# Kernel optimization log

Hardware: AMD Instinct MI355X
Metric: run time of the kernel (lower is better)

The kernel has to match this reference:

```python
import jax, jax.numpy as jnp
import numpy as np

TOPK = 2048


def setup_inputs() -> dict:
    key = jax.random.key(0)
    ks = jax.random.split(key, 16)
    M = 20000
    boxes = jax.random.uniform(ks[0], (M, 4), dtype=jnp.float32)
    scores = jax.random.uniform(ks[1], (M,), dtype=jnp.float32)
    classes = jax.random.randint(ks[2], (M,), 0, 80, dtype=jnp.int64)
    def lin(k, fan_in, fan_out):
        b = 1.0 / np.sqrt(fan_in)
        kw, kb = jax.random.split(k)
        w = jax.random.uniform(kw, (fan_in, fan_out), jnp.float32, -b, b)
        bias = jax.random.uniform(kb, (fan_out,), jnp.float32, -b, b)
        return w, bias
    sup_w1, sup_b1 = lin(ks[3], 7, 32)
    sup_w2, sup_b2 = lin(ks[4], 32, 16)
    sup_w3, sup_b3 = lin(ks[5], 16, 1)
    lam_w1, lam_b1 = lin(ks[6], 5, 16)
    lam_w2, lam_b2 = lin(ks[7], 16, 1)
    return {
        'boxes': boxes, 'scores': scores, 'classes': classes,
        'sup_w1': sup_w1, 'sup_b1': sup_b1, 'sup_w2': sup_w2, 'sup_b2': sup_b2,
        'sup_w3': sup_w3, 'sup_b3': sup_b3,
        'lam_w1': lam_w1, 'lam_b1': lam_b1, 'lam_w2': lam_w2, 'lam_b2': lam_b2,
    }


def _box_iou(b):
    # b: [N,4] in (x, y, w, h)
    x, y, w, h = b[:, 0], b[:, 1], b[:, 2], b[:, 3]
    area = w * h
    ix1 = jnp.maximum(x[:, None], x[None, :])
    iy1 = jnp.maximum(y[:, None], y[None, :])
    ix2 = jnp.minimum((x + w)[:, None], (x + w)[None, :])
    iy2 = jnp.minimum((y + h)[:, None], (y + h)[None, :])
    inter = jnp.clip(ix2 - ix1, 0) * jnp.clip(iy2 - iy1, 0)
    union = area[:, None] + area[None, :] - inter
    return inter / (union + 1e-06)


def _dacs(boxes, scores, classes,
          sup_w1, sup_b1, sup_w2, sup_b2, sup_w3, sup_b3,
          lam_w1, lam_b1, lam_w2, lam_b2):
    k = min(TOPK, scores.shape[0])
    top_scores, idx = jax.lax.top_k(scores, k)
    b = boxes[idx]            # [N,4]
    cls = classes[idx]        # [N]
    N = k
    iou = _box_iou(b)         # [N,N]
    D = iou.mean(axis=1)      # [N]
    x, y, w, h = b[:, 0], b[:, 1], b[:, 2], b[:, 3]
    feats = jnp.stack([
        iou,
        jnp.abs(x[:, None] - x[None, :]),
        jnp.abs(y[:, None] - y[None, :]),
        jnp.abs(w[:, None] - w[None, :]),
        jnp.abs(h[:, None] - h[None, :]),
        jnp.broadcast_to(top_scores[:, None], (N, N)),
        jnp.broadcast_to(top_scores[None, :], (N, N)),
    ], axis=-1)               # [N,N,7]
    hdn = jax.nn.relu(feats @ sup_w1 + sup_b1)       # [N,N,32]
    hdn = jax.nn.relu(hdn @ sup_w2 + sup_b2)         # [N,N,16]
    s_ij = jax.nn.sigmoid((hdn @ sup_w3 + sup_b3)[..., 0])  # [N,N]
    class_mask = (cls[:, None] == cls[None, :]).astype(s_ij.dtype)
    s_ij = s_ij * class_mask
    lam_in = jnp.concatenate([b, top_scores[:, None]], axis=1)  # [N,5]
    lam_h = jax.nn.relu(lam_in @ lam_w1 + lam_b1)
    lam = jax.nn.sigmoid((lam_h @ lam_w2 + lam_b2)[:, 0])       # [N]
    S = jnp.sum(s_ij * iou, axis=1)
    E = lam * S * D
    new_scores = top_scores * jnp.exp(-E)
    return b, new_scores, cls


def reference(boxes, scores, classes,
              sup_w1, sup_b1, sup_w2, sup_b2, sup_w3, sup_b3,
              lam_w1, lam_b1, lam_w2, lam_b2):
    return _dacs(boxes, scores, classes,
                 sup_w1, sup_b1, sup_w2, sup_b2, sup_w3, sup_b3,
                 lam_w1, lam_b1, lam_w2, lam_b2)
```

## Files before the change

### kernel.cpp

```cpp
#include <hip/hip_runtime.h>
#include <math.h>

#define TOPK 2048
#define NCLS 80
#define NBIN 4096
#define CMAX 2560
#define K1B  32
#define STN  1024
#define CTN  256
#define CROWS 2

struct SelP {
    const float* scores; const float* boxes; const int* classes;
    int M; int K;
    float4* sel_box; float* sel_score; int* sel_cls;
    int* cstart;
    short* clist;
};

struct CmpP {
    const float4* sel_box; const float* sel_score; const int* sel_cls;
    const int* cstart; const short* clist;
    const float* sw1; const float* sb1; const float* sw2; const float* sb2;
    const float* sw3; const float* sb3;
    const float* lw1; const float* lb1; const float* lw2; const float* lb2;
    int K;
    float* out_boxes; float* out_scores; float* out_cls;
};

__device__ __forceinline__ float iou_of(float xi, float yi, float ai,
                                        float x2i, float y2i, float4 bj) {
    float ix1 = fmaxf(xi, bj.x), iy1 = fmaxf(yi, bj.y);
    float ix2 = fminf(x2i, bj.x + bj.z), iy2 = fminf(y2i, bj.y + bj.w);
    float iw = fmaxf(ix2 - ix1, 0.0f), ih = fmaxf(iy2 - iy1, 0.0f);
    float inter = iw * ih;
    float uni = ai + bj.z * bj.w - inter;
    return inter / (uni + 1e-6f);
}

__device__ __forceinline__ int digest12(float s) {
    int v = (int)(s * 4096.0f);
    return v < 0 ? 0 : (v > NBIN - 1 ? NBIN - 1 : v);
}

__device__ __forceinline__ float key_score(unsigned long long kk) {
    unsigned mono = (unsigned)(kk >> 32);
    unsigned ob = (mono & 0x80000000u) ? (mono & 0x7FFFFFFFu) : ~mono;
    return __uint_as_float(ob);
}

__global__ __launch_bounds__(STN, 1) void k_sel(SelP p) {
    __shared__ int   bincur[NBIN];
    __shared__ int   binbase[NBIN];
    __shared__ unsigned long long skeys[CMAX];
    __shared__ int   sfx[STN];
    __shared__ int   wsum[STN / 64];
    __shared__ int   sh_cT;
    __shared__ int   cls_of[CMAX];
    __shared__ int   rk_of[CMAX];
    __shared__ int   ccnt[NCLS], ccur[NCLS];
    __shared__ int   wtot;

    int tid = threadIdx.x, bid = blockIdx.x;
    int M = p.M, K = p.K, M4 = M >> 2;
    bool prep = (bid == 0);

    for (int b = tid; b < NBIN; b += STN) bincur[b] = 0;
    if (tid < NCLS) ccnt[tid] = 0;
    __syncthreads();

    const float4* s4p = (const float4*)p.scores;
    for (int i4 = tid; i4 < M4; i4 += STN) {
        float4 v = s4p[i4];
        atomicAdd(&bincur[digest12(v.x)], 1);
        atomicAdd(&bincur[digest12(v.y)], 1);
        atomicAdd(&bincur[digest12(v.z)], 1);
        atomicAdd(&bincur[digest12(v.w)], 1);
    }
    for (int i = M4 * 4 + tid; i < M; i += STN)
        atomicAdd(&bincur[digest12(p.scores[i])], 1);
    __syncthreads();

    {
        const int BPT = NBIN / STN;
        int c0 = tid * BPT, sum = 0;
        #pragma unroll
        for (int u = 0; u < BPT; u++) sum += bincur[c0 + u];
        int lane = tid & 63;
        int x = sum;
        #pragma unroll
        for (int off = 1; off < 64; off <<= 1) {
            int v = __shfl_down(x, off, 64);
            if (lane + off < 64) x += v;
        }
        if (lane == 0) wsum[tid >> 6] = x;
        __syncthreads();
        if (tid < STN / 64) {
            int t = wsum[tid];
            #pragma unroll
            for (int off = 1; off < STN / 64; off <<= 1) {
                int v = __shfl_down(t, off, 64);
                if (tid + off < STN / 64) t += v;
            }
            wsum[tid] = t;
        }
        __syncthreads();
        int wid = tid >> 6;
        int higher = (wid < STN / 64 - 1) ? wsum[wid + 1] : 0;
        sfx[tid] = x + higher;
    }
    __syncthreads();

    {
        const int BPT = NBIN / STN;
        int running = (tid < STN - 1) ? sfx[tid + 1] : 0;
        int c0 = tid * BPT;
        for (int u = BPT - 1; u >= 0; u--) {
            int b = c0 + u, cnt = bincur[b];
            binbase[b] = running;
            if (running < K && running + cnt >= K) sh_cT = b;
            running += cnt;
        }
    }
    __syncthreads();
    int cT = sh_cT;
    for (int b = tid; b < NBIN; b += STN) bincur[b] = binbase[b];
    __syncthreads();

    for (int i4 = tid; i4 < M4; i4 += STN) {
        float4 v = s4p[i4];
        #pragma unroll
        for (int u = 0; u < 4; u++) {
            float s = (u == 0) ? v.x : (u == 1) ? v.y : (u == 2) ? v.z : v.w;
            int d = digest12(s);
            if (d >= cT) {
                int i = i4 * 4 + u;
                int slot = atomicAdd(&bincur[d], 1);
                if (slot < CMAX) {
                    unsigned b = __float_as_uint(s);
                    b = (b & 0x80000000u) ? ~b : (b | 0x80000000u);
                    skeys[slot] = ((unsigned long long)b << 32) |
                                  (unsigned long long)(0xFFFFFFFFu - (unsigned)i);
                }
            }
        }
    }
    for (int i = M4 * 4 + tid; i < M; i += STN) {
        float s = p.scores[i];
        int d = digest12(s);
        if (d >= cT) {
            int slot = atomicAdd(&bincur[d], 1);
            if (slot < CMAX) {
                unsigned b = __float_as_uint(s);
                b = (b & 0x80000000u) ? ~b : (b | 0x80000000u);
                skeys[slot] = ((unsigned long long)b << 32) |
                              (unsigned long long)(0xFFFFFFFFu - (unsigned)i);
            }
        }
    }
    __syncthreads();

    int C = bincur[cT]; if (C > CMAX) C = CMAX;
    {
        const float4* boxes4 = (const float4*)p.boxes;
        for (int s = tid; s < C; s += STN) {
            unsigned long long ks = skeys[s];
            unsigned idx = 0xFFFFFFFFu - (unsigned)(ks & 0xFFFFFFFFull);
            bool mine = ((int)(idx & (K1B - 1)) == bid);
            if (!prep && !mine) continue;
            float sc = key_score(ks);
            int d = digest12(sc);
            int st = binbase[d], en = bincur[d]; if (en > CMAX) en = CMAX;
            int r = binbase[d];
            for (int t = st; t < en; t++) r += (skeys[t] > ks) ? 1 : 0;
            bool ok = (r < K);
            int c = -1;
            if (ok) c = p.classes[idx];
            if (prep) {
                cls_of[s] = ok ? c : -1;
                rk_of[s] = r;
                if (ok) atomicAdd(&ccnt[c], 1);
            }
            if (mine && ok) {
                p.sel_box[r] = boxes4[idx];
                p.sel_score[r] = sc;
                p.sel_cls[r] = c;
            }
        }
    }
    __syncthreads();

    if (prep) {
        int x = 0, v = 0;
        if (tid < 128) {
            v = (tid < NCLS) ? ccnt[tid] : 0;
            x = v;
            #pragma unroll
            for (int off = 1; off < 64; off <<= 1) {
                int t = __shfl_up(x, off, 64);
                if ((tid & 63) >= off) x += t;
            }
            if (tid == 63) wtot = x;
        }
        __syncthreads();
        if (tid < NCLS) {
            int excl = x - v + ((tid >= 64) ? wtot : 0);
            ccur[tid] = excl;
            p.cstart[tid] = excl;
        }
        if (tid == 0) p.cstart[NCLS] = K;
        __syncthreads();
        for (int s = tid; s < C; s += STN) {
            int c = cls_of[s];
            if (c >= 0) {
                int pos = atomicAdd(&ccur[c], 1);
                p.clist[pos] = (short)rk_of[s];
            }
        }
    }
}

__global__ __launch_bounds__(CTN, 2) void k_cmp(CmpP p) {
    __shared__ float swt[914];
    __shared__ float wpart[8];
    __shared__ int   rowc[CROWS];
    __shared__ int   prefix[CROWS + 1];
    __shared__ float Ssum[CROWS], Drow[CROWS];

    int tid = threadIdx.x, bid = blockIdx.x;
    int K = p.K;
    int r0 = bid * CROWS;
    int nrows = K - r0; if (nrows > CROWS) nrows = CROWS;
    if (nrows <= 0) return;

    for (int t = tid; t < 224; t += CTN) swt[t] = p.sw1[t];
    if (tid < 32) swt[224 + tid] = p.sb1[tid];
    for (int t = tid; t < 512; t += CTN) swt[256 + t] = p.sw2[t];
    if (tid < 16) swt[768 + tid] = p.sb2[tid];
    if (tid < 16) swt[784 + tid] = p.sw3[tid];
    if (tid == 0) swt[800] = p.sb3[0];
    if (tid < 80) swt[801 + tid] = p.lw1[tid];
    if (tid < 16) swt[881 + tid] = p.lb1[tid];
    if (tid < 16) swt[897 + tid] = p.lw2[tid];
    if (tid == 0) swt[913] = p.lb2[0];

    if (tid < CROWS) {
        Ssum[tid] = 0.0f;
        int st = 0, cnt = 0;
        if (tid < nrows) {
            int c = p.sel_cls[r0 + tid];
            st = p.cstart[c];
            cnt = p.cstart[c + 1] - st;
        }
        rowc[tid] = st;
        prefix[tid] = cnt;
    }
    __syncthreads();
    if (tid == 0) {
        int a0 = prefix[0], a1 = prefix[1];
        prefix[0] = 0; prefix[1] = a0; prefix[2] = a0 + a1;
    }

    {
        float4 bi0 = p.sel_box[r0];
        float4 bi1 = (nrows > 1) ? p.sel_box[r0 + 1] : bi0;
        float a0 = bi0.z * bi0.w, x20 = bi0.x + bi0.z, y20 = bi0.y + bi0.w;
        float a1 = bi1.z * bi1.w, x21 = bi1.x + bi1.z, y21 = bi1.y + bi1.w;
        float d0 = 0.0f, d1 = 0.0f;
        for (int j = tid; j < K; j += CTN) {
            float4 bj = p.sel_box[j];
            d0 += iou_of(bi0.x, bi0.y, a0, x20, y20, bj);
            d1 += iou_of(bi1.x, bi1.y, a1, x21, y21, bj);
        }
        #pragma unroll
        for (int off = 32; off >= 1; off >>= 1) {
            d0 += __shfl_xor(d0, off, 64);
            d1 += __shfl_xor(d1, off, 64);
        }
        int lane = tid & 63, wv = tid >> 6;
        if (lane == 0) { wpart[wv * 2] = d0; wpart[wv * 2 + 1] = d1; }
    }
    __syncthreads();
    if (tid < nrows)
        Drow[tid] = (wpart[tid] + wpart[2 + tid] + wpart[4 + tid] + wpart[6 + tid])
                    / (float)K;

    int Pb = prefix[CROWS];
    const float* W1 = swt;       const float* B1 = swt + 224;
    const float* W2 = swt + 256; const float* B2 = swt + 768;
    const float* W3 = swt + 784; float B3 = swt[800];

    for (int pp = tid; pp < Pb; pp += CTN) {
        int row = (pp >= prefix[1]) ? 1 : 0;
        int j = (int)p.clist[rowc[row] + (pp - prefix[row])];
        float4 bi = p.sel_box[r0 + row];
        float4 bj = p.sel_box[j];
        float ai = bi.z * bi.w, x2i = bi.x + bi.z, y2i = bi.y + bi.w;
        float iou = iou_of(bi.x, bi.y, ai, x2i, y2i, bj);
        float f1 = fabsf(bi.x - bj.x), f2 = fabsf(bi.y - bj.y);
        float f3 = fabsf(bi.z - bj.z), f4 = fabsf(bi.w - bj.w);
        float f5 = p.sel_score[r0 + row], f6 = p.sel_score[j];
        float acc2[16];
        #pragma unroll
        for (int q = 0; q < 16; q++) acc2[q] = B2[q];
        #pragma unroll 2
        for (int o = 0; o < 32; o++) {
            float a = B1[o];
            a += iou * W1[0 * 32 + o];
            a += f1 * W1[1 * 32 + o];
            a += f2 * W1[2 * 32 + o];
            a += f3 * W1[3 * 32 + o];
            a += f4 * W1[4 * 32 + o];
            a += f5 * W1[5 * 32 + o];
            a += f6 * W1[6 * 32 + o];
            float h = fmaxf(a, 0.0f);
            #pragma unroll
            for (int q = 0; q < 16; q++) acc2[q] += h * W2[o * 16 + q];
        }
        float acc3 = B3;
        #pragma unroll
        for (int q = 0; q < 16; q++) acc3 += fmaxf(acc2[q], 0.0f) * W3[q];
        atomicAdd(&Ssum[row], iou / (1.0f + expf(-acc3)));
    }
    __syncthreads();

    if (tid < nrows) {
        int r = r0 + tid;
        float4 bi = p.sel_box[r];
        float si = p.sel_score[r];
        const float* LW1 = swt + 801; const float* LB1 = swt + 881;
        const float* LW2 = swt + 897; float LB2 = swt[913];
        float in5[5] = { bi.x, bi.y, bi.z, bi.w, si };
        float acc = LB2;
        #pragma unroll
        for (int o = 0; o < 16; o++) {
            float a2 = LB1[o];
            #pragma unroll
            for (int f = 0; f < 5; f++) a2 += in5[f] * LW1[f * 16 + o];
            acc += fmaxf(a2, 0.0f) * LW2[o];
        }
        float lam = 1.0f / (1.0f + expf(-acc));
        ((float4*)p.out_boxes)[r] = bi;
        p.out_cls[r] = (float)p.sel_cls[r];
        p.out_scores[r] = si * expf(-lam * Ssum[tid] * Drow[tid]);
    }
}

extern "C" void kernel_launch(void* const* d_in, const int* in_sizes, int n_in,
                              void* d_out, int out_size, void* d_ws, size_t ws_size,
                              hipStream_t stream) {
    int M = in_sizes[1];
    int K = (M < TOPK) ? M : TOPK;

    char* ws = (char*)d_ws;
    float4* sel_box   = (float4*)ws;           ws += (size_t)TOPK * 16;
    float*  sel_score = (float*)ws;            ws += (size_t)TOPK * 4;
    int*    sel_cls   = (int*)ws;              ws += (size_t)TOPK * 4;
    int*    cstart    = (int*)ws;              ws += (size_t)(NCLS + 2) * 4;
    short*  clist     = (short*)ws;            ws += (size_t)TOPK * 2;

    SelP sp;
    sp.scores  = (const float*)d_in[1];
    sp.boxes   = (const float*)d_in[0];
    sp.classes = (const int*)d_in[2];
    sp.M = M; sp.K = K;
    sp.sel_box = sel_box; sp.sel_score = sel_score; sp.sel_cls = sel_cls;
    sp.cstart = cstart; sp.clist = clist;

    CmpP cp;
    cp.sel_box = sel_box; cp.sel_score = sel_score; cp.sel_cls = sel_cls;
    cp.cstart = cstart; cp.clist = clist;
    cp.sw1 = (const float*)d_in[3];  cp.sb1 = (const float*)d_in[4];
    cp.sw2 = (const float*)d_in[5];  cp.sb2 = (const float*)d_in[6];
    cp.sw3 = (const float*)d_in[7];  cp.sb3 = (const float*)d_in[8];
    cp.lw1 = (const float*)d_in[9];  cp.lb1 = (const float*)d_in[10];
    cp.lw2 = (const float*)d_in[11]; cp.lb2 = (const float*)d_in[12];
    cp.K = K;
    cp.out_boxes  = (float*)d_out;
    cp.out_scores = (float*)d_out + (size_t)K * 4;
    cp.out_cls    = (float*)d_out + (size_t)K * 5;

    k_sel<<<K1B, STN, 0, stream>>>(sp);
    k_cmp<<<(K + CROWS - 1) / CROWS, CTN, 0, stream>>>(cp);
}
```

Measured before the change: 106.8 us.

## Collapse top-k selection to one block and process four rows per compute block

```diff
diff --git a/kernel.cpp b/kernel.cpp
--- a/kernel.cpp
+++ b/kernel.cpp
@@ -5,21 +5,20 @@
 #define NCLS 80
 #define NBIN 4096
 #define CMAX 2560
-#define K1B  32
-#define STN  1024
-#define CTN  256
-#define CROWS 2
+#define TNS  1024
+#define TND  512
+#define CROWS 4
 
 struct SelP {
     const float* scores; const float* boxes; const int* classes;
     int M; int K;
-    float4* sel_box; float* sel_score; int* sel_cls;
+    float4* selB; float* selS; int* selC;
     int* cstart;
     short* clist;
 };
 
 struct CmpP {
-    const float4* sel_box; const float* sel_score; const int* sel_cls;
+    const float4* selB; const float* selS; const int* selC;
     const int* cstart; const short* clist;
     const float* sw1; const float* sb1; const float* sw2; const float* sb2;
     const float* sw3; const float* sb3;
@@ -43,46 +42,50 @@
     return v < 0 ? 0 : (v > NBIN - 1 ? NBIN - 1 : v);
 }
 
+__device__ __forceinline__ unsigned long long make_key(float s, unsigned i) {
+    unsigned b = __float_as_uint(s);
+    b = (b & 0x80000000u) ? ~b : (b | 0x80000000u);
+    return ((unsigned long long)b << 32) |
+           (unsigned long long)(0xFFFFFFFFu - i);
+}
+
 __device__ __forceinline__ float key_score(unsigned long long kk) {
     unsigned mono = (unsigned)(kk >> 32);
     unsigned ob = (mono & 0x80000000u) ? (mono & 0x7FFFFFFFu) : ~mono;
     return __uint_as_float(ob);
 }
 
-__global__ __launch_bounds__(STN, 1) void k_sel(SelP p) {
+__global__ __launch_bounds__(TNS, 1) void k_sel(SelP p) {
     __shared__ int   bincur[NBIN];
-    __shared__ int   binbase[NBIN];
     __shared__ unsigned long long skeys[CMAX];
-    __shared__ int   sfx[STN];
-    __shared__ int   wsum[STN / 64];
+    __shared__ int   sfx[TNS];
+    __shared__ int   wsum[TNS / 64];
     __shared__ int   sh_cT;
-    __shared__ int   cls_of[CMAX];
-    __shared__ int   rk_of[CMAX];
+    __shared__ short scls[TOPK];
     __shared__ int   ccnt[NCLS], ccur[NCLS];
     __shared__ int   wtot;
 
-    int tid = threadIdx.x, bid = blockIdx.x;
+    int tid = threadIdx.x;
     int M = p.M, K = p.K, M4 = M >> 2;
-    bool prep = (bid == 0);
-
-    for (int b = tid; b < NBIN; b += STN) bincur[b] = 0;
+
+    for (int b = tid; b < NBIN; b += TNS) bincur[b] = 0;
     if (tid < NCLS) ccnt[tid] = 0;
     __syncthreads();
 
     const float4* s4p = (const float4*)p.scores;
-    for (int i4 = tid; i4 < M4; i4 += STN) {
+    for (int i4 = tid; i4 < M4; i4 += TNS) {
         float4 v = s4p[i4];
         atomicAdd(&bincur[digest12(v.x)], 1);
         atomicAdd(&bincur[digest12(v.y)], 1);
         atomicAdd(&bincur[digest12(v.z)], 1);
         atomicAdd(&bincur[digest12(v.w)], 1);
     }
-    for (int i = M4 * 4 + tid; i < M; i += STN)
+    for (int i = M4 * 4 + tid; i < M; i += TNS)
         atomicAdd(&bincur[digest12(p.scores[i])], 1);
     __syncthreads();
 
     {
-        const int BPT = NBIN / STN;
+        const int BPT = NBIN / TNS;
         int c0 = tid * BPT, sum = 0;
         #pragma unroll
         for (int u = 0; u < BPT; u++) sum += bincur[c0 + u];
@@ -95,102 +98,89 @@
         }
         if (lane == 0) wsum[tid >> 6] = x;
         __syncthreads();
-        if (tid < STN / 64) {
+        if (tid < TNS / 64) {
             int t = wsum[tid];
             #pragma unroll
-            for (int off = 1; off < STN / 64; off <<= 1) {
+            for (int off = 1; off < TNS / 64; off <<= 1) {
                 int v = __shfl_down(t, off, 64);
-                if (tid + off < STN / 64) t += v;
+                if (tid + off < TNS / 64) t += v;
             }
             wsum[tid] = t;
         }
         __syncthreads();
         int wid = tid >> 6;
-        int higher = (wid < STN / 64 - 1) ? wsum[wid + 1] : 0;
+        int higher = (wid < TNS / 64 - 1) ? wsum[wid + 1] : 0;
         sfx[tid] = x + higher;
     }
     __syncthreads();
 
     {
-        const int BPT = NBIN / STN;
-        int running = (tid < STN - 1) ? sfx[tid + 1] : 0;
+        const int BPT = NBIN / TNS;
+        int running = (tid < TNS - 1) ? sfx[tid + 1] : 0;
         int c0 = tid * BPT;
         for (int u = BPT - 1; u >= 0; u--) {
             int b = c0 + u, cnt = bincur[b];
-            binbase[b] = running;
             if (running < K && running + cnt >= K) sh_cT = b;
+            bincur[b] = (running << 16);
             running += cnt;
         }
     }
     __syncthreads();
     int cT = sh_cT;
-    for (int b = tid; b < NBIN; b += STN) bincur[b] = binbase[b];
-    __syncthreads();
-
-    for (int i4 = tid; i4 < M4; i4 += STN) {
+
+    for (int i4 = tid; i4 < M4; i4 += TNS) {
         float4 v = s4p[i4];
         #pragma unroll
         for (int u = 0; u < 4; u++) {
             float s = (u == 0) ? v.x : (u == 1) ? v.y : (u == 2) ? v.z : v.w;
             int d = digest12(s);
             if (d >= cT) {
-                int i = i4 * 4 + u;
-                int slot = atomicAdd(&bincur[d], 1);
-                if (slot < CMAX) {
-                    unsigned b = __float_as_uint(s);
-                    b = (b & 0x80000000u) ? ~b : (b | 0x80000000u);
-                    skeys[slot] = ((unsigned long long)b << 32) |
-                                  (unsigned long long)(0xFFFFFFFFu - (unsigned)i);
-                }
+                int old = atomicAdd(&bincur[d], 1);
+                int slot = (old >> 16) + (old & 0xFFFF);
+                if (slot < CMAX)
+                    skeys[slot] = make_key(s, (unsigned)(i4 * 4 + u));
             }
         }
     }
-    for (int i = M4 * 4 + tid; i < M; i += STN) {
+    for (int i = M4 * 4 + tid; i < M; i += TNS) {
         float s = p.scores[i];
         int d = digest12(s);
         if (d >= cT) {
-            int slot = atomicAdd(&bincur[d], 1);
-            if (slot < CMAX) {
-                unsigned b = __float_as_uint(s);
-                b = (b & 0x80000000u) ? ~b : (b | 0x80000000u);
-                skeys[slot] = ((unsigned long long)b << 32) |
-                              (unsigned long long)(0xFFFFFFFFu - (unsigned)i);
-            }
-        }
-    }
-    __syncthreads();
-
-    int C = bincur[cT]; if (C > CMAX) C = CMAX;
+            int old = atomicAdd(&bincur[d], 1);
+            int slot = (old >> 16) + (old & 0xFFFF);
+            if (slot < CMAX) skeys[slot] = make_key(s, (unsigned)i);
+        }
+    }
+    __syncthreads();
+
+    int pkT = bincur[cT];
+    int C = (pkT >> 16) + (pkT & 0xFFFF); if (C > CMAX) C = CMAX;
     {
         const float4* boxes4 = (const float4*)p.boxes;
-        for (int s = tid; s < C; s += STN) {
+        for (int s = tid; s < C; s += TNS) {
             unsigned long long ks = skeys[s];
             unsigned idx = 0xFFFFFFFFu - (unsigned)(ks & 0xFFFFFFFFull);
-            bool mine = ((int)(idx & (K1B - 1)) == bid);
-            if (!prep && !mine) continue;
             float sc = key_score(ks);
             int d = digest12(sc);
-            int st = binbase[d], en = bincur[d]; if (en > CMAX) en = CMAX;
-            int r = binbase[d];
+            int pk = bincur[d];
+            int st = pk >> 16;
+            int en = st + (pk & 0xFFFF); if (en > CMAX) en = CMAX;
+            int r = st;
             for (int t = st; t < en; t++) r += (skeys[t] > ks) ? 1 : 0;
-            bool ok = (r < K);
-            int c = -1;
-            if (ok) c = p.classes[idx];
-            if (prep) {
-                cls_of[s] = ok ? c : -1;
-                rk_of[s] = r;
-                if (ok) atomicAdd(&ccnt[c], 1);
+            if (r < K) {
+                int c = p.classes[idx];
+                p.selB[r] = boxes4[idx];
+                p.selS[r] = sc;
+                p.selC[r] = c;
+                scls[r] = (short)c;
             }
-            if (mine && ok) {
-                p.sel_box[r] = boxes4[idx];
-                p.sel_score[r] = sc;
-                p.sel_cls[r] = c;
-            }
-        }
-    }
-    __syncthreads();
-
-    if (prep) {
+        }
+    }
+    __syncthreads();
+
+    for (int r = tid; r < K; r += TNS) atomicAdd(&ccnt[scls[r]], 1);
+    __syncthreads();
+    {
         int x = 0, v = 0;
         if (tid < 128) {
             v = (tid < NCLS) ? ccnt[tid] : 0;
@@ -210,19 +200,16 @@
         }
         if (tid == 0) p.cstart[NCLS] = K;
         __syncthreads();
-        for (int s = tid; s < C; s += STN) {
-            int c = cls_of[s];
-            if (c >= 0) {
-                int pos = atomicAdd(&ccur[c], 1);
-                p.clist[pos] = (short)rk_of[s];
-            }
-        }
-    }
-}
-
-__global__ __launch_bounds__(CTN, 2) void k_cmp(CmpP p) {
+        for (int r = tid; r < K; r += TNS) {
+            int pos = atomicAdd(&ccur[scls[r]], 1);
+            p.clist[pos] = (short)r;
+        }
+    }
+}
+
+__global__ __launch_bounds__(TND, 4) void k_cmp(CmpP p) {
     __shared__ float swt[914];
-    __shared__ float wpart[8];
+    __shared__ float wpart[(TND / 64) * CROWS];
     __shared__ int   rowc[CROWS];
     __shared__ int   prefix[CROWS + 1];
     __shared__ float Ssum[CROWS], Drow[CROWS];
@@ -233,9 +220,9 @@
     int nrows = K - r0; if (nrows > CROWS) nrows = CROWS;
     if (nrows <= 0) return;
 
-    for (int t = tid; t < 224; t += CTN) swt[t] = p.sw1[t];
+    for (int t = tid; t < 224; t += TND) swt[t] = p.sw1[t];
     if (tid < 32) swt[224 + tid] = p.sb1[tid];
-    for (int t = tid; t < 512; t += CTN) swt[256 + t] = p.sw2[t];
+    for (int t = tid; t < 512; t += TND) swt[256 + t] = p.sw2[t];
     if (tid < 16) swt[768 + tid] = p.sb2[tid];
     if (tid < 16) swt[784 + tid] = p.sw3[tid];
     if (tid == 0) swt[800] = p.sb3[0];
@@ -248,7 +235,7 @@
         Ssum[tid] = 0.0f;
         int st = 0, cnt = 0;
         if (tid < nrows) {
-            int c = p.sel_cls[r0 + tid];
+            int c = p.selC[r0 + tid];
             st = p.cstart[c];
             cnt = p.cstart[c + 1] - st;
         }
@@ -257,49 +244,67 @@
     }
     __syncthreads();
     if (tid == 0) {
-        int a0 = prefix[0], a1 = prefix[1];
-        prefix[0] = 0; prefix[1] = a0; prefix[2] = a0 + a1;
-    }
-
-    {
-        float4 bi0 = p.sel_box[r0];
-        float4 bi1 = (nrows > 1) ? p.sel_box[r0 + 1] : bi0;
-        float a0 = bi0.z * bi0.w, x20 = bi0.x + bi0.z, y20 = bi0.y + bi0.w;
-        float a1 = bi1.z * bi1.w, x21 = bi1.x + bi1.z, y21 = bi1.y + bi1.w;
-        float d0 = 0.0f, d1 = 0.0f;
-        for (int j = tid; j < K; j += CTN) {
-            float4 bj = p.sel_box[j];
-            d0 += iou_of(bi0.x, bi0.y, a0, x20, y20, bj);
-            d1 += iou_of(bi1.x, bi1.y, a1, x21, y21, bj);
+        int acc = 0;
+        #pragma unroll
+        for (int rr = 0; rr < CROWS; rr++) { int t = prefix[rr]; prefix[rr] = acc; acc += t; }
+        prefix[CROWS] = acc;
+    }
+
+    {
+        float4 b0 = p.selB[r0];
+        float4 b1 = (nrows > 1) ? p.selB[r0 + 1] : b0;
+        float4 b2 = (nrows > 2) ? p.selB[r0 + 2] : b0;
+        float4 b3 = (nrows > 3) ? p.selB[r0 + 3] : b0;
+        float a0 = b0.z * b0.w, x20 = b0.x + b0.z, y20 = b0.y + b0.w;
+        float a1 = b1.z * b1.w, x21 = b1.x + b1.z, y21 = b1.y + b1.w;
+        float a2 = b2.z * b2.w, x22 = b2.x + b2.z, y22 = b2.y + b2.w;
+        float a3 = b3.z * b3.w, x23 = b3.x + b3.z, y23 = b3.y + b3.w;
+        float d0 = 0.0f, d1 = 0.0f, d2 = 0.0f, d3 = 0.0f;
+        for (int j = tid; j < K; j += TND) {
+            float4 bj = p.selB[j];
+            d0 += iou_of(b0.x, b0.y, a0, x20, y20, bj);
+            d1 += iou_of(b1.x, b1.y, a1, x21, y21, bj);
+            d2 += iou_of(b2.x, b2.y, a2, x22, y22, bj);
+            d3 += iou_of(b3.x, b3.y, a3, x23, y23, bj);
         }
         #pragma unroll
         for (int off = 32; off >= 1; off >>= 1) {
             d0 += __shfl_xor(d0, off, 64);
             d1 += __shfl_xor(d1, off, 64);
+            d2 += __shfl_xor(d2, off, 64);
+            d3 += __shfl_xor(d3, off, 64);
         }
         int lane = tid & 63, wv = tid >> 6;
-        if (lane == 0) { wpart[wv * 2] = d0; wpart[wv * 2 + 1] = d1; }
-    }
-    __syncthreads();
-    if (tid < nrows)
-        Drow[tid] = (wpart[tid] + wpart[2 + tid] + wpart[4 + tid] + wpart[6 + tid])
-                    / (float)K;
+        if (lane == 0) {
+            wpart[wv * CROWS + 0] = d0;
+            wpart[wv * CROWS + 1] = d1;
+            wpart[wv * CROWS + 2] = d2;
+            wpart[wv * CROWS + 3] = d3;
+        }
+    }
+    __syncthreads();
+    if (tid < nrows) {
+        float s = 0.0f;
+        #pragma unroll
+        for (int wv = 0; wv < TND / 64; wv++) s += wpart[wv * CROWS + tid];
+        Drow[tid] = s / (float)K;
+    }
 
     int Pb = prefix[CROWS];
     const float* W1 = swt;       const float* B1 = swt + 224;
     const float* W2 = swt + 256; const float* B2 = swt + 768;
     const float* W3 = swt + 784; float B3 = swt[800];
 
-    for (int pp = tid; pp < Pb; pp += CTN) {
-        int row = (pp >= prefix[1]) ? 1 : 0;
+    for (int pp = tid; pp < Pb; pp += TND) {
+        int row = (pp >= prefix[1]) + (pp >= prefix[2]) + (pp >= prefix[3]);
         int j = (int)p.clist[rowc[row] + (pp - prefix[row])];
-        float4 bi = p.sel_box[r0 + row];
-        float4 bj = p.sel_box[j];
+        float4 bi = p.selB[r0 + row];
+        float4 bj = p.selB[j];
         float ai = bi.z * bi.w, x2i = bi.x + bi.z, y2i = bi.y + bi.w;
         float iou = iou_of(bi.x, bi.y, ai, x2i, y2i, bj);
         float f1 = fabsf(bi.x - bj.x), f2 = fabsf(bi.y - bj.y);
         float f3 = fabsf(bi.z - bj.z), f4 = fabsf(bi.w - bj.w);
-        float f5 = p.sel_score[r0 + row], f6 = p.sel_score[j];
+        float f5 = p.selS[r0 + row], f6 = p.selS[j];
         float acc2[16];
         #pragma unroll
         for (int q = 0; q < 16; q++) acc2[q] = B2[q];
@@ -326,8 +331,8 @@
 
     if (tid < nrows) {
         int r = r0 + tid;
-        float4 bi = p.sel_box[r];
-        float si = p.sel_score[r];
+        float4 bi = p.selB[r];
+        float si = p.selS[r];
         const float* LW1 = swt + 801; const float* LB1 = swt + 881;
         const float* LW2 = swt + 897; float LB2 = swt[913];
         float in5[5] = { bi.x, bi.y, bi.z, bi.w, si };
@@ -341,7 +346,7 @@
         }
         float lam = 1.0f / (1.0f + expf(-acc));
         ((float4*)p.out_boxes)[r] = bi;
-        p.out_cls[r] = (float)p.sel_cls[r];
+        p.out_cls[r] = (float)p.selC[r];
         p.out_scores[r] = si * expf(-lam * Ssum[tid] * Drow[tid]);
     }
 }
@@ -353,22 +358,22 @@
     int K = (M < TOPK) ? M : TOPK;
 
     char* ws = (char*)d_ws;
-    float4* sel_box   = (float4*)ws;           ws += (size_t)TOPK * 16;
-    float*  sel_score = (float*)ws;            ws += (size_t)TOPK * 4;
-    int*    sel_cls   = (int*)ws;              ws += (size_t)TOPK * 4;
-    int*    cstart    = (int*)ws;              ws += (size_t)(NCLS + 2) * 4;
-    short*  clist     = (short*)ws;            ws += (size_t)TOPK * 2;
+    float4* selB   = (float4*)ws;              ws += (size_t)TOPK * 16;
+    float*  selS   = (float*)ws;               ws += (size_t)TOPK * 4;
+    int*    selC   = (int*)ws;                 ws += (size_t)TOPK * 4;
+    int*    cstart = (int*)ws;                 ws += (size_t)(NCLS + 2) * 4;
+    short*  clist  = (short*)ws;               ws += (size_t)TOPK * 2;
 
     SelP sp;
     sp.scores  = (const float*)d_in[1];
     sp.boxes   = (const float*)d_in[0];
     sp.classes = (const int*)d_in[2];
     sp.M = M; sp.K = K;
-    sp.sel_box = sel_box; sp.sel_score = sel_score; sp.sel_cls = sel_cls;
+    sp.selB = selB; sp.selS = selS; sp.selC = selC;
     sp.cstart = cstart; sp.clist = clist;
 
     CmpP cp;
-    cp.sel_box = sel_box; cp.sel_score = sel_score; cp.sel_cls = sel_cls;
+    cp.selB = selB; cp.selS = selS; cp.selC = selC;
     cp.cstart = cstart; cp.clist = clist;
     cp.sw1 = (const float*)d_in[3];  cp.sb1 = (const float*)d_in[4];
     cp.sw2 = (const float*)d_in[5];  cp.sb2 = (const float*)d_in[6];
@@ -380,6 +385,6 @@
     cp.out_scores = (float*)d_out + (size_t)K * 4;
     cp.out_cls    = (float*)d_out + (size_t)K * 5;
 
-    k_sel<<<K1B, STN, 0, stream>>>(sp);
-    k_cmp<<<(K + CROWS - 1) / CROWS, CTN, 0, stream>>>(cp);
-}
+    k_sel<<<1, TNS, 0, stream>>>(sp);
+    k_cmp<<<(K + CROWS - 1) / CROWS, TND, 0, stream>>>(cp);
+}
```

After: 105.7 us. About the same (-1.0%).
